# Optimization experiments

Measured on AMD Instinct MI355X. Metric: run time of the kernel, lower is better.

## Reference

```python
import jax, jax.numpy as jnp
import numpy as np


def setup_inputs() -> dict:
    key = jax.random.key(0)
    ks = jax.random.split(key, 4)
    B, C, H, W = 8, 256, 64, 64
    x = jax.random.normal(ks[0], (B, C, H, W), dtype=jnp.float32)
    Wq = jax.random.normal(ks[1], (C, C), dtype=jnp.float32) * 0.02
    Wk = jax.random.normal(ks[2], (C, C), dtype=jnp.float32) * 0.02
    Wv = jax.random.normal(ks[3], (C, C), dtype=jnp.float32) * 0.02
    bq = jnp.zeros((C,), dtype=jnp.float32)
    bk = jnp.zeros((C,), dtype=jnp.float32)
    bv = jnp.zeros((C,), dtype=jnp.float32)
    gamma = jnp.float32(0.5)  # learned scalar (torch init is 0.0; nonzero here for a nontrivial output)
    return {"x": x, "Wq": Wq, "bq": bq, "Wk": Wk, "bk": bk, "Wv": Wv, "bv": bv, "gamma": gamma}


def reference(x, Wq, bq, Wk, bk, Wv, bv, gamma):
    B, C, H, W = x.shape
    N = H * W
    f = x.reshape(B, C, N)  # flatten spatial tokens
    # 1x1 Conv1d == per-token linear: out[b,d,n] = sum_c W[d,c] * f[b,c,n] + b[d]
    q = jnp.einsum('dc,bcn->bdn', Wq, f) + bq[:, None]  # [B, C, N]
    k = jnp.einsum('dc,bcn->bdn', Wk, f) + bk[:, None]  # [B, C, N]
    v = jnp.einsum('dc,bcn->bdn', Wv, f) + bv[:, None]  # [B, C, N]
    # query_key[b, n, m] = sum_c q[b,c,n] * k[b,c,m], divided by width W (shape[-1], NOT N)
    qk = jnp.einsum('bcn,bcm->bnm', q, k) / W  # [B, N, N]
    # softmax over dim=1 => over the QUERY-token axis (SAGAN quirk)
    attn = jax.nn.softmax(qk, axis=1)
    # out[b,c,m] = sum_n v[b,c,n] * attn[b,n,m]
    o = jnp.einsum('bcn,bnm->bcm', v, attn).reshape(B, C, H, W)
    return gamma * o + x
```

## Files before the change

kernel.cpp:

```cpp
#include <hip/hip_runtime.h>

typedef __bf16 bf16_t;
typedef __bf16 bf16x8 __attribute__((ext_vector_type(8)));
typedef float f32x16 __attribute__((ext_vector_type(16)));

#define NB 8
#define NC 256
#define NN 4096

__device__ __forceinline__ f32x16 mfma32(bf16x8 a, bf16x8 b, f32x16 c) {
  return __builtin_amdgcn_mfma_f32_32x32x16_bf16(a, b, c, 0, 0, 0);
}

__device__ __forceinline__ f32x16 mfma8(uint2 a, uint2 b, f32x16 c) {
  union { uint2 u; long long l; } A, B;
  A.u = a; B.u = b;
  return __builtin_amdgcn_mfma_f32_32x32x16_fp8_fp8(A.l, B.l, c, 0, 0, 0);
}

__device__ __forceinline__ void gload_lds16(const void* g, void* l) {
  __builtin_amdgcn_global_load_lds((const __attribute__((address_space(1))) void*)g,
                                   (__attribute__((address_space(3))) void*)l, 16, 0, 0);
}

__device__ __forceinline__ unsigned int packbf2(float lo, float hi) {
  union { bf16_t h; unsigned short s; } a, b;
  a.h = (bf16_t)lo; b.h = (bf16_t)hi;
  return (unsigned int)a.s | ((unsigned int)b.s << 16);
}

__device__ __forceinline__ f32x16 fzero() {
  f32x16 z;
#pragma unroll
  for (int r = 0; r < 16; r++) z[r] = 0.f;
  return z;
}

#define QSCALE (0.015625f * 1.44269504088896f)

__global__ void kconv_w(const float* __restrict__ Wq, const float* __restrict__ bq,
                        const float* __restrict__ Wk, const float* __restrict__ bk,
                        const float* __restrict__ Wv, const float* __restrict__ bv,
                        bf16_t* __restrict__ Wc, float* __restrict__ bc) {
  int idx = blockIdx.x * 256 + threadIdx.x;
  int d = idx >> 8;
  float w;
  if (d < 256)      w = Wq[idx];
  else if (d < 512) w = Wk[idx - 65536];
  else              w = Wv[idx - 131072];
  Wc[idx] = (bf16_t)w;
  if (idx < 768) {
    float v = idx < 256 ? bq[idx] : (idx < 512 ? bk[idx - 256] : bv[idx - 512]);
    bc[idx] = v;
  }
}

__global__ void ktranspose(const float* __restrict__ x, bf16_t* __restrict__ fT) {
  __shared__ float tile[64][65];
  int bid = blockIdx.x;
  int b = bid >> 8;
  int r = bid & 255;
  int n0 = (r >> 2) * 64;
  int c0 = (r & 3) * 64;
  int t = threadIdx.x;
  const float* xb = x + ((long)b * NC + c0) * NN + n0;
  int lr = t >> 4;
  int lc = (t & 15) * 4;
#pragma unroll
  for (int i = 0; i < 4; i++) {
    float4 v4 = *(const float4*)(xb + (long)(lr + i * 16) * NN + lc);
    tile[lr + i * 16][lc + 0] = v4.x; tile[lr + i * 16][lc + 1] = v4.y;
    tile[lr + i * 16][lc + 2] = v4.z; tile[lr + i * 16][lc + 3] = v4.w;
  }
  __syncthreads();
  int nl = t >> 2;
  int cc = (t & 3) * 16;
  bf16_t* dst = fT + ((long)b * NN + n0 + nl) * NC + c0 + cc;
  union { bf16_t h[8]; uint4 u; } p0, p1;
#pragma unroll
  for (int j = 0; j < 8; j++) p0.h[j] = (bf16_t)tile[cc + j][nl];
#pragma unroll
  for (int j = 0; j < 8; j++) p1.h[j] = (bf16_t)tile[cc + 8 + j][nl];
  *(uint4*)dst = p0.u;
  *(uint4*)(dst + 8) = p1.u;
}

__global__ __launch_bounds__(256) void kproj(const bf16_t* __restrict__ Wc, const float* __restrict__ bc,
                                             const bf16_t* __restrict__ fT,
                                             unsigned char* __restrict__ qT8, unsigned char* __restrict__ kT8,
                                             unsigned char* __restrict__ vO8) {
  __shared__ bf16_t ft[128 * 256];
  int bid = blockIdx.x;
  int mt = bid % 6;
  int nb = bid / 6;
  int d0 = mt * 128;
  int gc0 = nb * 128;
  int b = gc0 >> 12;
  int n0 = gc0 & 4095;
  int t = threadIdx.x, lane = t & 63, w = t >> 6;
  int lm = lane & 31, g = lane >> 5;
  const bf16_t* ftb = fT + ((long)b * NN + n0) * NC;
#pragma unroll
  for (int i2 = 0; i2 < 16; i2++) {
    int call = w * 16 + i2;
    int p = call * 1024 + lane * 16;
    int n = p >> 9, cb = p & 511;
    int scb = cb ^ ((n & 7) << 4);
    gload_lds16(ftb + (long)n * NC + (scb >> 1), (char*)ft + call * 1024);
  }
  __syncthreads();

  f32x16 acc00 = fzero(), acc01 = fzero(), acc10 = fzero(), acc11 = fzero();
  int dbase = d0 + (w >> 1) * 64;
  int nbase = (w & 1) * 64;
  const bf16_t* wr = Wc + (long)dbase * NC;
#pragma unroll
  for (int j = 0; j < 16; j++) {
    int cc = j * 16 + g * 8;
    bf16x8 a0 = *(const bf16x8*)(wr + (long)lm * NC + cc);
    bf16x8 a1 = *(const bf16x8*)(wr + (long)(lm + 32) * NC + cc);
    int row0 = nbase + lm;
    bf16x8 b0 = *(const bf16x8*)((char*)ft + row0 * 512 + ((cc * 2) ^ ((row0 & 7) << 4)));
    int row1 = row0 + 32;
    bf16x8 b1 = *(const bf16x8*)((char*)ft + row1 * 512 + ((cc * 2) ^ ((row1 & 7) << 4)));
    acc00 = mfma32(a0, b0, acc00);
    acc01 = mfma32(a0, b1, acc01);
    acc10 = mfma32(a1, b0, acc10);
    acc11 = mfma32(a1, b1, acc11);
  }

  auto epi = [&](f32x16 a, int dt, int nt2) {
    int db = dbase + dt * 32;
    int colg = n0 + nbase + nt2 * 32 + lm;
    long ntile = (long)b * 128 + (colg >> 5);
    int n5 = colg & 31;
    if (mt >= 4) {
      long nidx = ntile * 8192 + (n5 >> 4) * 512 +
                  ((n5 >> 2) & 1) * 256 + ((n5 & 3) + ((n5 & 8) >> 1));
#pragma unroll
      for (int r = 0; r < 16; r++) {
        int d = db + (r & 3) + 8 * (r >> 2) + 4 * g;
        int c = d - 512;
        unsigned int f8 = __builtin_amdgcn_cvt_pk_fp8_f32(a[r] + bc[d], 0.f, 0, false);
        vO8[nidx + (c >> 5) * 1024 + (c & 31) * 8] = (unsigned char)f8;
      }
    } else if (mt < 2) {
      long base = ntile * 8192 + lm * 8;
#pragma unroll
      for (int t4 = 0; t4 < 4; t4++) {
        int cb = db + 8 * t4 + 4 * g;
        unsigned int pk = __builtin_amdgcn_cvt_pk_fp8_f32(a[4 * t4 + 0] + bc[cb + 0],
                                                          a[4 * t4 + 1] + bc[cb + 1], 0, false);
        pk = __builtin_amdgcn_cvt_pk_fp8_f32(a[4 * t4 + 2] + bc[cb + 2],
                                             a[4 * t4 + 3] + bc[cb + 3], pk, true);
        *(unsigned int*)(qT8 + base + (cb >> 4) * 512 + ((cb >> 3) & 1) * 256 + (cb & 7)) = pk;
      }
    } else {
      unsigned char* dst = kT8 + ((long)b * NN + colg) * 256 - 256;
#pragma unroll
      for (int r2 = 0; r2 < 8; r2++) {
        int r = r2 * 2;
        int d = db + (r & 3) + 8 * (r >> 2) + 4 * g;
        unsigned int pk = __builtin_amdgcn_cvt_pk_fp8_f32(a[r] + bc[d], a[r + 1] + bc[d + 1], 0, false);
        *(unsigned short*)(dst + d) = (unsigned short)pk;
      }
    }
  };
  epi(acc00, 0, 0); epi(acc01, 0, 1); epi(acc10, 1, 0); epi(acc11, 1, 1);
}

__global__ __launch_bounds__(256, 2) void kattn(const unsigned char* __restrict__ qT8,
                                                const unsigned char* __restrict__ kT8,
                                                const unsigned char* __restrict__ vO8,
                                                char* __restrict__ R0, char* __restrict__ R1, int iters) {
  __shared__ unsigned char Kt[2][8192];
  __shared__ unsigned char Vt[2][8192];
  int bid = blockIdx.x;
  int b = bid & 7;
  int mtile = (bid >> 3) & 31;
  int split = bid >> 8;
  int nt0 = split * iters, ntE = nt0 + iters;
  int t = threadIdx.x, lane = t & 63, w = t >> 6;
  int lm = lane & 31, g = lane >> 5;
  int mw = mtile * 128 + w * 32;
  const unsigned char* qb = qT8 + (long)b * 1048576;
  const unsigned char* vtb = vO8 + (long)b * 1048576;

  uint2 qf[16];
  const unsigned char* kb = kT8 + ((long)b * NN + mw + lm) * 256 + g * 8;
#pragma unroll
  for (int j = 0; j < 16; j++) qf[j] = *(const uint2*)(kb + j * 16);

  f32x16 acc[8];
#pragma unroll
  for (int ct = 0; ct < 8; ct++) acc[ct] = fzero();
  float lsum = 0.f;

  auto stageK = [&](int nt, int bufi) {
    const unsigned char* src0 = qb + (long)nt * 8192;
#pragma unroll
    for (int i = 0; i < 2; i++) {
      int call = w * 2 + i;
      gload_lds16(src0 + call * 1024 + lane * 16, &Kt[bufi][call * 1024]);
    }
  };
  auto stageV = [&](int nt, int bufi) {
    const unsigned char* src0 = vtb + (long)nt * 8192;
#pragma unroll
    for (int i = 0; i < 2; i++) {
      int call = w * 2 + i;
      gload_lds16(src0 + call * 1024 + lane * 16, &Vt[bufi][call * 1024]);
    }
  };

  stageK(nt0, 0);
  stageV(nt0, 0);
  __syncthreads();

  int buf = 0;
  for (int nt = nt0; nt < ntE; nt++) {
    bool more = nt + 1 < ntE;
    if (more) { stageK(nt + 1, buf ^ 1); stageV(nt + 1, buf ^ 1); }
    __builtin_amdgcn_s_setprio(1);
    const unsigned char* kbase = &Kt[buf][0] + lane * 8;
    f32x16 sa = fzero(), sb = fzero();
#pragma unroll
    for (int j = 0; j < 8; j++) {
      uint2 ka = *(const uint2*)(kbase + (2 * j) * 512);
      sa = mfma8(ka, qf[2 * j], sa);
      uint2 kc = *(const uint2*)(kbase + (2 * j + 1) * 512);
      sb = mfma8(kc, qf[2 * j + 1], sb);
    }
    __builtin_amdgcn_s_setprio(0);
    float s[16];
#pragma unroll
    for (int r = 0; r < 16; r++) s[r] = __builtin_amdgcn_exp2f((sa[r] + sb[r]) * QSCALE);
    lsum += (((s[0] + s[1]) + (s[2] + s[3])) + ((s[4] + s[5]) + (s[6] + s[7]))) +
            (((s[8] + s[9]) + (s[10] + s[11])) + ((s[12] + s[13]) + (s[14] + s[15])));
    uint2 pf0, pf1;
    pf0.x = __builtin_amdgcn_cvt_pk_fp8_f32(s[0], s[1], 0, false);
    pf0.x = __builtin_amdgcn_cvt_pk_fp8_f32(s[2], s[3], pf0.x, true);
    pf0.y = __builtin_amdgcn_cvt_pk_fp8_f32(s[4], s[5], 0, false);
    pf0.y = __builtin_amdgcn_cvt_pk_fp8_f32(s[6], s[7], pf0.y, true);
    pf1.x = __builtin_amdgcn_cvt_pk_fp8_f32(s[8], s[9], 0, false);
    pf1.x = __builtin_amdgcn_cvt_pk_fp8_f32(s[10], s[11], pf1.x, true);
    pf1.y = __builtin_amdgcn_cvt_pk_fp8_f32(s[12], s[13], 0, false);
    pf1.y = __builtin_amdgcn_cvt_pk_fp8_f32(s[14], s[15], pf1.y, true);
    __builtin_amdgcn_s_setprio(1);
    const unsigned char* vbase = &Vt[buf][0] + g * 256 + lm * 8;
#pragma unroll
    for (int ct = 0; ct < 8; ct++) {
      uint2 va = *(const uint2*)(vbase + ct * 1024);
      acc[ct] = mfma8(va, pf0, acc[ct]);
    }
#pragma unroll
    for (int ct = 0; ct < 8; ct++) {
      uint2 vb2 = *(const uint2*)(vbase + ct * 1024 + 512);
      acc[ct] = mfma8(vb2, pf1, acc[ct]);
    }
    __builtin_amdgcn_s_setprio(0);
    __syncthreads();
    buf ^= 1;
  }
  float ltot = lsum + __shfl_xor(lsum, 32, 64);
  char* R = split ? R1 : R0;
  unsigned int* PP = (unsigned int*)R;
  float* MLf = (float*)(R + 16777216);
  int mg = ((b * 32 + mtile) << 2) + w;
  if (lane < 32) MLf[mg * 32 + lm] = ltot;
#pragma unroll
  for (int ct = 0; ct < 8; ct++)
#pragma unroll
    for (int r2 = 0; r2 < 8; r2++) {
      unsigned int pk = packbf2(acc[ct][2 * r2], acc[ct][2 * r2 + 1]);
      PP[(((mg << 3) + ct) * 8 + r2) * 64 + lane] = pk;
    }
}

__global__ __launch_bounds__(256) void kcombine(const char* __restrict__ R0, const char* __restrict__ R1,
                                                int nsplit, const float* __restrict__ x,
                                                const float* __restrict__ gma, float* __restrict__ out) {
  int tid = blockIdx.x * 256 + threadIdx.x;
  const unsigned int* P0 = (const unsigned int*)R0;
  const float* ML0 = (const float*)(R0 + 16777216);
  int lane = tid & 63, lm = lane & 31, g = lane >> 5;
  int r2 = (tid >> 6) & 7, ct = (tid >> 9) & 7, mg = tid >> 12;
  int b = mg >> 7, mtile = (mg >> 2) & 31, w = mg & 3;
  int m = mtile * 128 + w * 32 + lm;
  int c0 = ct * 32 + 2 * (r2 & 1) + 8 * (r2 >> 1) + 4 * g;
  unsigned int p0 = P0[tid];
  float ox = __uint_as_float(p0 << 16);
  float oy = __uint_as_float(p0 & 0xffff0000u);
  float L = ML0[mg * 32 + lm];
  if (nsplit == 2) {
    const unsigned int* P1 = (const unsigned int*)R1;
    const float* ML1 = (const float*)(R1 + 16777216);
    unsigned int p1 = P1[tid];
    ox += __uint_as_float(p1 << 16);
    oy += __uint_as_float(p1 & 0xffff0000u);
    L += ML1[mg * 32 + lm];
  }
  float sc = gma[0] / L;
  long o0 = ((long)(b * NC + c0)) * NN + m;
  out[o0] = ox * sc + x[o0];
  out[o0 + NN] = oy * sc + x[o0 + NN];
}

extern "C" void kernel_launch(void* const* d_in, const int* in_sizes, int n_in,
                              void* d_out, int out_size, void* d_ws, size_t ws_size,
                              hipStream_t stream) {
  const float* x   = (const float*)d_in[0];
  const float* Wq  = (const float*)d_in[1];
  const float* bq  = (const float*)d_in[2];
  const float* Wk  = (const float*)d_in[3];
  const float* bk  = (const float*)d_in[4];
  const float* Wv  = (const float*)d_in[5];
  const float* bv  = (const float*)d_in[6];
  const float* gma = (const float*)d_in[7];
  float* out = (float*)d_out;
  char* ws = (char*)d_ws;
  unsigned char* qT8 = (unsigned char*)(ws);
  unsigned char* kT8 = (unsigned char*)(ws + 8388608);
  unsigned char* vO8 = (unsigned char*)(ws + 16777216);
  bf16_t* fT = (bf16_t*)(ws + 25165824);
  bf16_t* Wc = (bf16_t*)(ws + 41943040);
  float*  bc = (float*)(ws + 42336256);
  char* R0 = ws + 25165824;
  char* R1 = ws + 42340352;
  size_t need2 = 42340352 + 16908288;
  int nsplit = (ws_size >= need2) ? 2 : 1;

  kconv_w<<<768, 256, 0, stream>>>(Wq, bq, Wk, bk, Wv, bv, Wc, bc);
  ktranspose<<<2048, 256, 0, stream>>>(x, fT);
  kproj<<<1536, 256, 0, stream>>>(Wc, bc, fT, qT8, kT8, vO8);
  kattn<<<256 * nsplit, 256, 0, stream>>>(qT8, kT8, vO8, R0, R1, 128 / nsplit);
  kcombine<<<16384, 256, 0, stream>>>(R0, R1, nsplit, x, gma, out);
}
```

Baseline: 191.4 us.

## Software-pipeline QK and PV across tiles with interleaved MFMA bursts

Restructures the attention loop so the QK^T MFMAs for tile i+1 run interleaved with the PV MFMAs for tile i, and K staging runs one tile ahead of V staging. The exp/convert softmax step then overlaps with matrix work instead of stalling the MFMA pipe between two dependent phases. The loop is unrolled by two with explicit prologue and epilogue and drops the setprio hints. It assumes iters is even and at least 2, and keeps two sets of P fragments live, which adds register pressure.

```diff
diff --git a/kernel.cpp b/kernel.cpp
--- a/kernel.cpp
+++ b/kernel.cpp
@@ -179,7 +179,7 @@
   int b = bid & 7;
   int mtile = (bid >> 3) & 31;
   int split = bid >> 8;
-  int nt0 = split * iters, ntE = nt0 + iters;
+  int nt0 = split * iters;
   int t = threadIdx.x, lane = t & 63, w = t >> 6;
   int lm = lane & 31, g = lane >> 5;
   int mw = mtile * 128 + w * 32;
@@ -195,35 +195,27 @@
 #pragma unroll
   for (int ct = 0; ct < 8; ct++) acc[ct] = fzero();
   float lsum = 0.f;
-
-  auto stageK = [&](int nt, int bufi) {
-    const unsigned char* src0 = qb + (long)nt * 8192;
-#pragma unroll
-    for (int i = 0; i < 2; i++) {
-      int call = w * 2 + i;
+  f32x16 sa, sb;
+
+  auto stageK = [&](int i, int bufi) {
+    const unsigned char* src0 = qb + (long)(nt0 + i) * 8192;
+#pragma unroll
+    for (int ii = 0; ii < 2; ii++) {
+      int call = w * 2 + ii;
       gload_lds16(src0 + call * 1024 + lane * 16, &Kt[bufi][call * 1024]);
     }
   };
-  auto stageV = [&](int nt, int bufi) {
-    const unsigned char* src0 = vtb + (long)nt * 8192;
-#pragma unroll
-    for (int i = 0; i < 2; i++) {
-      int call = w * 2 + i;
+  auto stageV = [&](int i, int bufi) {
+    const unsigned char* src0 = vtb + (long)(nt0 + i) * 8192;
+#pragma unroll
+    for (int ii = 0; ii < 2; ii++) {
+      int call = w * 2 + ii;
       gload_lds16(src0 + call * 1024 + lane * 16, &Vt[bufi][call * 1024]);
     }
   };
-
-  stageK(nt0, 0);
-  stageV(nt0, 0);
-  __syncthreads();
-
-  int buf = 0;
-  for (int nt = nt0; nt < ntE; nt++) {
-    bool more = nt + 1 < ntE;
-    if (more) { stageK(nt + 1, buf ^ 1); stageV(nt + 1, buf ^ 1); }
-    __builtin_amdgcn_s_setprio(1);
-    const unsigned char* kbase = &Kt[buf][0] + lane * 8;
-    f32x16 sa = fzero(), sb = fzero();
+  auto qkonly = [&](int kbuf) {
+    const unsigned char* kbase = &Kt[kbuf][0] + lane * 8;
+    sa = fzero(); sb = fzero();
 #pragma unroll
     for (int j = 0; j < 8; j++) {
       uint2 ka = *(const uint2*)(kbase + (2 * j) * 512);
@@ -231,37 +223,80 @@
       uint2 kc = *(const uint2*)(kbase + (2 * j + 1) * 512);
       sb = mfma8(kc, qf[2 * j + 1], sb);
     }
-    __builtin_amdgcn_s_setprio(0);
+  };
+  auto burst = [&](int kbuf, int vbuf, uint2 p0, uint2 p1) {
+    const unsigned char* kbase = &Kt[kbuf][0] + lane * 8;
+    const unsigned char* vbase = &Vt[vbuf][0] + g * 256 + lm * 8;
+    sa = fzero(); sb = fzero();
+#pragma unroll
+    for (int u = 0; u < 8; u++) {
+      uint2 ka = *(const uint2*)(kbase + (2 * u) * 512);
+      sa = mfma8(ka, qf[2 * u], sa);
+      uint2 va = *(const uint2*)(vbase + u * 1024);
+      acc[u] = mfma8(va, p0, acc[u]);
+      uint2 kc = *(const uint2*)(kbase + (2 * u + 1) * 512);
+      sb = mfma8(kc, qf[2 * u + 1], sb);
+      uint2 vb2 = *(const uint2*)(vbase + u * 1024 + 512);
+      acc[u] = mfma8(vb2, p1, acc[u]);
+    }
+  };
+  auto pvonly = [&](int vbuf, uint2 p0, uint2 p1) {
+    const unsigned char* vbase = &Vt[vbuf][0] + g * 256 + lm * 8;
+#pragma unroll
+    for (int u = 0; u < 8; u++) {
+      uint2 va = *(const uint2*)(vbase + u * 1024);
+      acc[u] = mfma8(va, p0, acc[u]);
+      uint2 vb2 = *(const uint2*)(vbase + u * 1024 + 512);
+      acc[u] = mfma8(vb2, p1, acc[u]);
+    }
+  };
+  auto smax = [&](uint2& p0, uint2& p1) {
     float s[16];
 #pragma unroll
     for (int r = 0; r < 16; r++) s[r] = __builtin_amdgcn_exp2f((sa[r] + sb[r]) * QSCALE);
     lsum += (((s[0] + s[1]) + (s[2] + s[3])) + ((s[4] + s[5]) + (s[6] + s[7]))) +
             (((s[8] + s[9]) + (s[10] + s[11])) + ((s[12] + s[13]) + (s[14] + s[15])));
-    uint2 pf0, pf1;
-    pf0.x = __builtin_amdgcn_cvt_pk_fp8_f32(s[0], s[1], 0, false);
-    pf0.x = __builtin_amdgcn_cvt_pk_fp8_f32(s[2], s[3], pf0.x, true);
-    pf0.y = __builtin_amdgcn_cvt_pk_fp8_f32(s[4], s[5], 0, false);
-    pf0.y = __builtin_amdgcn_cvt_pk_fp8_f32(s[6], s[7], pf0.y, true);
-    pf1.x = __builtin_amdgcn_cvt_pk_fp8_f32(s[8], s[9], 0, false);
-    pf1.x = __builtin_amdgcn_cvt_pk_fp8_f32(s[10], s[11], pf1.x, true);
-    pf1.y = __builtin_amdgcn_cvt_pk_fp8_f32(s[12], s[13], 0, false);
-    pf1.y = __builtin_amdgcn_cvt_pk_fp8_f32(s[14], s[15], pf1.y, true);
-    __builtin_amdgcn_s_setprio(1);
-    const unsigned char* vbase = &Vt[buf][0] + g * 256 + lm * 8;
-#pragma unroll
-    for (int ct = 0; ct < 8; ct++) {
-      uint2 va = *(const uint2*)(vbase + ct * 1024);
-      acc[ct] = mfma8(va, pf0, acc[ct]);
-    }
-#pragma unroll
-    for (int ct = 0; ct < 8; ct++) {
-      uint2 vb2 = *(const uint2*)(vbase + ct * 1024 + 512);
-      acc[ct] = mfma8(vb2, pf1, acc[ct]);
-    }
-    __builtin_amdgcn_s_setprio(0);
+    p0.x = __builtin_amdgcn_cvt_pk_fp8_f32(s[0], s[1], 0, false);
+    p0.x = __builtin_amdgcn_cvt_pk_fp8_f32(s[2], s[3], p0.x, true);
+    p0.y = __builtin_amdgcn_cvt_pk_fp8_f32(s[4], s[5], 0, false);
+    p0.y = __builtin_amdgcn_cvt_pk_fp8_f32(s[6], s[7], p0.y, true);
+    p1.x = __builtin_amdgcn_cvt_pk_fp8_f32(s[8], s[9], 0, false);
+    p1.x = __builtin_amdgcn_cvt_pk_fp8_f32(s[10], s[11], p1.x, true);
+    p1.y = __builtin_amdgcn_cvt_pk_fp8_f32(s[12], s[13], 0, false);
+    p1.y = __builtin_amdgcn_cvt_pk_fp8_f32(s[14], s[15], p1.y, true);
+  };
+
+  uint2 pfA0, pfA1, pfB0, pfB1;
+
+  stageK(0, 0);
+  __syncthreads();
+  stageK(1, 1);
+  stageV(0, 0);
+  qkonly(0);
+  smax(pfA0, pfA1);
+  __syncthreads();
+
+  int npairs = (iters - 2) >> 1;
+#pragma unroll 1
+  for (int ii = 0; ii < npairs; ii++) {
+    int i = 2 * ii + 1;
+    stageK(i + 1, 0);
+    stageV(i, 1);
+    burst(1, 0, pfA0, pfA1);
+    smax(pfB0, pfB1);
     __syncthreads();
-    buf ^= 1;
-  }
+    stageK(i + 2, 1);
+    stageV(i + 1, 0);
+    burst(0, 1, pfB0, pfB1);
+    smax(pfA0, pfA1);
+    __syncthreads();
+  }
+  stageV(iters - 1, 1);
+  burst(1, 0, pfA0, pfA1);
+  smax(pfB0, pfB1);
+  __syncthreads();
+  pvonly(1, pfB0, pfB1);
+
   float ltot = lsum + __shfl_xor(lsum, 32, 64);
   char* R = split ? R1 : R0;
   unsigned int* PP = (unsigned int*)R;
```

Measured after the change: 187.4 us. 1.02x faster.

## Switch attention kernel to 16x16x32 fp8 MFMA with 8 waves per block

Applied to the files above, without the earlier changes.

Replaces the 32x32x16 fp8 MFMA in the attention kernel with 16x16x32 fp8 MFMA, so each wave now handles 16 query columns instead of 32, and doubles the block to 512 threads (8 waves). Because the operand fragment layout differs, the projection epilogue that writes the fp8 Q and V tiles and the combine kernel's indexing are rewritten to match. Register pressure per wave drops (accumulators go from 8x16 to 16x4 floats and the Q fragments are halved), which is meant to raise occupancy and shorten dependency chains. In exchange each block issues more, smaller MFMAs, and more waves share each staged K/V tile.

```diff
diff --git a/kernel.cpp b/kernel.cpp
--- a/kernel.cpp
+++ b/kernel.cpp
@@ -3,6 +3,7 @@
 typedef __bf16 bf16_t;
 typedef __bf16 bf16x8 __attribute__((ext_vector_type(8)));
 typedef float f32x16 __attribute__((ext_vector_type(16)));
+typedef float f32x4 __attribute__((ext_vector_type(4)));
 
 #define NB 8
 #define NC 256
@@ -12,10 +13,10 @@
   return __builtin_amdgcn_mfma_f32_32x32x16_bf16(a, b, c, 0, 0, 0);
 }
 
-__device__ __forceinline__ f32x16 mfma8(uint2 a, uint2 b, f32x16 c) {
+__device__ __forceinline__ f32x4 mfma16(uint2 a, uint2 b, f32x4 c) {
   union { uint2 u; long long l; } A, B;
   A.u = a; B.u = b;
-  return __builtin_amdgcn_mfma_f32_32x32x16_fp8_fp8(A.l, B.l, c, 0, 0, 0);
+  return __builtin_amdgcn_mfma_f32_16x16x32_fp8_fp8(A.l, B.l, c, 0, 0, 0);
 }
 
 __device__ __forceinline__ void gload_lds16(const void* g, void* l) {
@@ -132,20 +133,24 @@
   auto epi = [&](f32x16 a, int dt, int nt2) {
     int db = dbase + dt * 32;
     int colg = n0 + nbase + nt2 * 32 + lm;
-    long ntile = (long)b * 128 + (colg >> 5);
+    long tb = ((long)b * 128 + (colg >> 5)) * 8192;
     int n5 = colg & 31;
     if (mt >= 4) {
-      long nidx = ntile * 8192 + (n5 >> 4) * 512 +
-                  ((n5 >> 2) & 1) * 256 + ((n5 & 3) + ((n5 & 8) >> 1));
+      int q5 = (n5 >> 2) & 3;
+      int e5 = ((n5 >> 4) << 2) + (n5 & 3);
+      int ct0 = (db - 512) >> 4;
 #pragma unroll
       for (int r = 0; r < 16; r++) {
         int d = db + (r & 3) + 8 * (r >> 2) + 4 * g;
-        int c = d - 512;
+        int ct = ct0 + (r >> 3);
+        int kq = (r & 3) + 8 * ((r >> 2) & 1) + 4 * g;
         unsigned int f8 = __builtin_amdgcn_cvt_pk_fp8_f32(a[r] + bc[d], 0.f, 0, false);
-        vO8[nidx + (c >> 5) * 1024 + (c & 31) * 8] = (unsigned char)f8;
+        vO8[tb + (ct * 64 + q5 * 16 + kq) * 8 + e5] = (unsigned char)f8;
       }
     } else if (mt < 2) {
-      long base = ntile * 8192 + lm * 8;
+      int h = (n5 >> 4) & 1;
+      int nr = n5 & 15;
+      int j = db >> 5;
 #pragma unroll
       for (int t4 = 0; t4 < 4; t4++) {
         int cb = db + 8 * t4 + 4 * g;
@@ -153,7 +158,7 @@
                                                           a[4 * t4 + 1] + bc[cb + 1], 0, false);
         pk = __builtin_amdgcn_cvt_pk_fp8_f32(a[4 * t4 + 2] + bc[cb + 2],
                                              a[4 * t4 + 3] + bc[cb + 3], pk, true);
-        *(unsigned int*)(qT8 + base + (cb >> 4) * 512 + ((cb >> 3) & 1) * 256 + (cb & 7)) = pk;
+        *(unsigned int*)(qT8 + tb + (j * 2 + h) * 512 + (t4 * 16 + nr) * 8 + 4 * g) = pk;
       }
     } else {
       unsigned char* dst = kT8 + ((long)b * NN + colg) * 256 - 256;
@@ -169,7 +174,7 @@
   epi(acc00, 0, 0); epi(acc01, 0, 1); epi(acc10, 1, 0); epi(acc11, 1, 1);
 }
 
-__global__ __launch_bounds__(256, 2) void kattn(const unsigned char* __restrict__ qT8,
+__global__ __launch_bounds__(512, 4) void kattn(const unsigned char* __restrict__ qT8,
                                                 const unsigned char* __restrict__ kT8,
                                                 const unsigned char* __restrict__ vO8,
                                                 char* __restrict__ R0, char* __restrict__ R1, int iters) {
@@ -181,36 +186,26 @@
   int split = bid >> 8;
   int nt0 = split * iters, ntE = nt0 + iters;
   int t = threadIdx.x, lane = t & 63, w = t >> 6;
-  int lm = lane & 31, g = lane >> 5;
-  int mw = mtile * 128 + w * 32;
+  int l4 = lane & 15, q = (lane >> 4) & 3;
+  int mw = mtile * 128 + w * 16;
   const unsigned char* qb = qT8 + (long)b * 1048576;
   const unsigned char* vtb = vO8 + (long)b * 1048576;
 
-  uint2 qf[16];
-  const unsigned char* kb = kT8 + ((long)b * NN + mw + lm) * 256 + g * 8;
-#pragma unroll
-  for (int j = 0; j < 16; j++) qf[j] = *(const uint2*)(kb + j * 16);
-
-  f32x16 acc[8];
-#pragma unroll
-  for (int ct = 0; ct < 8; ct++) acc[ct] = fzero();
+  uint2 qf[8];
+  const unsigned char* kb = kT8 + ((long)b * NN + mw + l4) * 256 + q * 8;
+#pragma unroll
+  for (int j = 0; j < 8; j++) qf[j] = *(const uint2*)(kb + j * 32);
+
+  f32x4 acc[16];
+#pragma unroll
+  for (int ct = 0; ct < 16; ct++) acc[ct] = f32x4{0.f, 0.f, 0.f, 0.f};
   float lsum = 0.f;
 
   auto stageK = [&](int nt, int bufi) {
-    const unsigned char* src0 = qb + (long)nt * 8192;
-#pragma unroll
-    for (int i = 0; i < 2; i++) {
-      int call = w * 2 + i;
-      gload_lds16(src0 + call * 1024 + lane * 16, &Kt[bufi][call * 1024]);
-    }
+    gload_lds16(qb + (long)nt * 8192 + w * 1024 + lane * 16, &Kt[bufi][w * 1024]);
   };
   auto stageV = [&](int nt, int bufi) {
-    const unsigned char* src0 = vtb + (long)nt * 8192;
-#pragma unroll
-    for (int i = 0; i < 2; i++) {
-      int call = w * 2 + i;
-      gload_lds16(src0 + call * 1024 + lane * 16, &Vt[bufi][call * 1024]);
-    }
+    gload_lds16(vtb + (long)nt * 8192 + w * 1024 + lane * 16, &Vt[bufi][w * 1024]);
   };
 
   stageK(nt0, 0);
@@ -223,58 +218,52 @@
     if (more) { stageK(nt + 1, buf ^ 1); stageV(nt + 1, buf ^ 1); }
     __builtin_amdgcn_s_setprio(1);
     const unsigned char* kbase = &Kt[buf][0] + lane * 8;
-    f32x16 sa = fzero(), sb = fzero();
+    f32x4 s0 = f32x4{0.f, 0.f, 0.f, 0.f}, s1 = f32x4{0.f, 0.f, 0.f, 0.f};
 #pragma unroll
     for (int j = 0; j < 8; j++) {
-      uint2 ka = *(const uint2*)(kbase + (2 * j) * 512);
-      sa = mfma8(ka, qf[2 * j], sa);
-      uint2 kc = *(const uint2*)(kbase + (2 * j + 1) * 512);
-      sb = mfma8(kc, qf[2 * j + 1], sb);
+      uint2 a0 = *(const uint2*)(kbase + (2 * j) * 512);
+      s0 = mfma16(a0, qf[j], s0);
+      uint2 a1 = *(const uint2*)(kbase + (2 * j + 1) * 512);
+      s1 = mfma16(a1, qf[j], s1);
     }
     __builtin_amdgcn_s_setprio(0);
-    float s[16];
-#pragma unroll
-    for (int r = 0; r < 16; r++) s[r] = __builtin_amdgcn_exp2f((sa[r] + sb[r]) * QSCALE);
-    lsum += (((s[0] + s[1]) + (s[2] + s[3])) + ((s[4] + s[5]) + (s[6] + s[7]))) +
-            (((s[8] + s[9]) + (s[10] + s[11])) + ((s[12] + s[13]) + (s[14] + s[15])));
-    uint2 pf0, pf1;
-    pf0.x = __builtin_amdgcn_cvt_pk_fp8_f32(s[0], s[1], 0, false);
-    pf0.x = __builtin_amdgcn_cvt_pk_fp8_f32(s[2], s[3], pf0.x, true);
-    pf0.y = __builtin_amdgcn_cvt_pk_fp8_f32(s[4], s[5], 0, false);
-    pf0.y = __builtin_amdgcn_cvt_pk_fp8_f32(s[6], s[7], pf0.y, true);
-    pf1.x = __builtin_amdgcn_cvt_pk_fp8_f32(s[8], s[9], 0, false);
-    pf1.x = __builtin_amdgcn_cvt_pk_fp8_f32(s[10], s[11], pf1.x, true);
-    pf1.y = __builtin_amdgcn_cvt_pk_fp8_f32(s[12], s[13], 0, false);
-    pf1.y = __builtin_amdgcn_cvt_pk_fp8_f32(s[14], s[15], pf1.y, true);
+    float e[8];
+#pragma unroll
+    for (int r = 0; r < 4; r++) {
+      e[r] = __builtin_amdgcn_exp2f(s0[r] * QSCALE);
+      e[4 + r] = __builtin_amdgcn_exp2f(s1[r] * QSCALE);
+    }
+    lsum += ((e[0] + e[1]) + (e[2] + e[3])) + ((e[4] + e[5]) + (e[6] + e[7]));
+    uint2 pf;
+    pf.x = __builtin_amdgcn_cvt_pk_fp8_f32(e[0], e[1], 0, false);
+    pf.x = __builtin_amdgcn_cvt_pk_fp8_f32(e[2], e[3], pf.x, true);
+    pf.y = __builtin_amdgcn_cvt_pk_fp8_f32(e[4], e[5], 0, false);
+    pf.y = __builtin_amdgcn_cvt_pk_fp8_f32(e[6], e[7], pf.y, true);
     __builtin_amdgcn_s_setprio(1);
-    const unsigned char* vbase = &Vt[buf][0] + g * 256 + lm * 8;
-#pragma unroll
-    for (int ct = 0; ct < 8; ct++) {
-      uint2 va = *(const uint2*)(vbase + ct * 1024);
-      acc[ct] = mfma8(va, pf0, acc[ct]);
-    }
-#pragma unroll
-    for (int ct = 0; ct < 8; ct++) {
-      uint2 vb2 = *(const uint2*)(vbase + ct * 1024 + 512);
-      acc[ct] = mfma8(vb2, pf1, acc[ct]);
+    const unsigned char* vbase = &Vt[buf][0] + lane * 8;
+#pragma unroll
+    for (int ct = 0; ct < 16; ct++) {
+      uint2 va = *(const uint2*)(vbase + ct * 512);
+      acc[ct] = mfma16(va, pf, acc[ct]);
     }
     __builtin_amdgcn_s_setprio(0);
     __syncthreads();
     buf ^= 1;
   }
-  float ltot = lsum + __shfl_xor(lsum, 32, 64);
+  float ltot = lsum + __shfl_xor(lsum, 16, 64);
+  ltot += __shfl_xor(ltot, 32, 64);
   char* R = split ? R1 : R0;
   unsigned int* PP = (unsigned int*)R;
   float* MLf = (float*)(R + 16777216);
-  int mg = ((b * 32 + mtile) << 2) + w;
-  if (lane < 32) MLf[mg * 32 + lm] = ltot;
-#pragma unroll
-  for (int ct = 0; ct < 8; ct++)
-#pragma unroll
-    for (int r2 = 0; r2 < 8; r2++) {
-      unsigned int pk = packbf2(acc[ct][2 * r2], acc[ct][2 * r2 + 1]);
-      PP[(((mg << 3) + ct) * 8 + r2) * 64 + lane] = pk;
-    }
+  int mg = ((b * 32 + mtile) << 3) + w;
+  if (lane < 16) MLf[mg * 16 + lane] = ltot;
+#pragma unroll
+  for (int ct = 0; ct < 16; ct++) {
+    uint2 pk;
+    pk.x = packbf2(acc[ct][0], acc[ct][1]);
+    pk.y = packbf2(acc[ct][2], acc[ct][3]);
+    *(uint2*)(PP + (mg * 16 + ct) * 128 + lane * 2) = pk;
+  }
 }
 
 __global__ __launch_bounds__(256) void kcombine(const char* __restrict__ R0, const char* __restrict__ R1,
@@ -283,22 +272,24 @@
   int tid = blockIdx.x * 256 + threadIdx.x;
   const unsigned int* P0 = (const unsigned int*)R0;
   const float* ML0 = (const float*)(R0 + 16777216);
-  int lane = tid & 63, lm = lane & 31, g = lane >> 5;
-  int r2 = (tid >> 6) & 7, ct = (tid >> 9) & 7, mg = tid >> 12;
-  int b = mg >> 7, mtile = (mg >> 2) & 31, w = mg & 3;
-  int m = mtile * 128 + w * 32 + lm;
-  int c0 = ct * 32 + 2 * (r2 & 1) + 8 * (r2 >> 1) + 4 * g;
+  int mg = tid >> 11;
+  int ct = (tid >> 7) & 15;
+  int lane = (tid >> 1) & 63;
+  int rr = tid & 1;
+  int b = mg >> 8, mtile = (mg >> 3) & 31, w = mg & 7;
+  int m = mtile * 128 + w * 16 + (lane & 15);
+  int c0 = ct * 16 + ((lane >> 4) & 3) * 4 + rr * 2;
   unsigned int p0 = P0[tid];
   float ox = __uint_as_float(p0 << 16);
   float oy = __uint_as_float(p0 & 0xffff0000u);
-  float L = ML0[mg * 32 + lm];
+  float L = ML0[mg * 16 + (lane & 15)];
   if (nsplit == 2) {
     const unsigned int* P1 = (const unsigned int*)R1;
     const float* ML1 = (const float*)(R1 + 16777216);
     unsigned int p1 = P1[tid];
     ox += __uint_as_float(p1 << 16);
     oy += __uint_as_float(p1 & 0xffff0000u);
-    L += ML1[mg * 32 + lm];
+    L += ML1[mg * 16 + (lane & 15)];
   }
   float sc = gma[0] / L;
   long o0 = ((long)(b * NC + c0)) * NN + m;
@@ -333,6 +324,6 @@
   kconv_w<<<768, 256, 0, stream>>>(Wq, bq, Wk, bk, Wv, bv, Wc, bc);
   ktranspose<<<2048, 256, 0, stream>>>(x, fT);
   kproj<<<1536, 256, 0, stream>>>(Wc, bc, fT, qT8, kT8, vO8);
-  kattn<<<256 * nsplit, 256, 0, stream>>>(qT8, kT8, vO8, R0, R1, 128 / nsplit);
+  kattn<<<256 * nsplit, 512, 0, stream>>>(qT8, kT8, vO8, R0, R1, 128 / nsplit);
   kcombine<<<16384, 256, 0, stream>>>(R0, R1, nsplit, x, gma, out);
 }
```

Measured after the change: 180.3 us. -5.8%, faster.
